# Performance work log

Measured on AMD Instinct MI355X. Metric: run time of the kernel, lower is better.

The kernel has to match this reference:

```python
import jax, jax.numpy as jnp
import numpy as np

N = 8192   # nodes
F = 16     # node features (col 0 = signal, last 3 = xyz)
H = 64     # hidden
G = 256    # number of graphs (segments)
EPS = 1e-3 # keras LayerNormalization default epsilon


def setup_inputs() -> dict:
    key = jax.random.key(0)
    ks = jax.random.split(key, 10)
    s = 0.05
    X = jax.random.normal(ks[0], (N, F), jnp.float32)
    # dense pre-normalized adjacency (spektral GCNConv expects normalized A)
    A = jax.random.uniform(ks[1], (N, N), jnp.float32) * (1.0 / N)
    I = jnp.sort(jax.random.randint(ks[2], (N,), 0, G)).astype(jnp.int32)
    W0 = jax.random.normal(ks[3], (F, H), jnp.float32) * s
    b0 = jnp.zeros((H,), jnp.float32)
    g0 = jnp.ones((H,), jnp.float32)
    be0 = jnp.zeros((H,), jnp.float32)
    W1 = jax.random.normal(ks[4], (H, H), jnp.float32) * s
    b1 = jnp.zeros((H,), jnp.float32)
    g1 = jnp.ones((H,), jnp.float32)
    be1 = jnp.zeros((H,), jnp.float32)
    Wf = jax.random.normal(ks[5], (H, H), jnp.float32) * s
    bf = jnp.zeros((H,), jnp.float32)
    Wa = jax.random.normal(ks[6], (H, H), jnp.float32) * s
    ba = jnp.zeros((H,), jnp.float32)
    Wout = jax.random.normal(ks[7], (H + 3, 3), jnp.float32) * s
    bout = jnp.zeros((3,), jnp.float32)
    return dict(X=X, A=A, I=I, W0=W0, b0=b0, g0=g0, be0=be0,
                W1=W1, b1=b1, g1=g1, be1=be1,
                Wf=Wf, bf=bf, Wa=Wa, ba=ba, Wout=Wout, bout=bout)


def _layer_norm(x, gamma, beta):
    m = jnp.mean(x, axis=-1, keepdims=True)
    v = jnp.mean(jnp.square(x - m), axis=-1, keepdims=True)
    return (x - m) * jax.lax.rsqrt(v + EPS) * gamma + beta


def reference(X, A, I, W0, b0, g0, be0, W1, b1, g1, be1, Wf, bf, Wa, ba, Wout, bout):
    I = I.astype(jnp.int32)
    # GCN layer 0: relu(A @ X @ W0 + b0) -> LayerNorm
    h0 = _layer_norm(jax.nn.relu(A @ (X @ W0) + b0), g0, be0)
    # GCN layer 1 + LayerNorm + residual (i > 0)
    h = _layer_norm(jax.nn.relu(A @ (h0 @ W1) + b1), g1, be1) + h0
    # GlobalAttentionPool: Dense features * sigmoid-gated attention, segment-summed per graph
    feat = h @ Wf + bf                       # [N, H]
    attn = jax.nn.sigmoid(h @ Wa + ba)       # [N, H]
    g = jax.ops.segment_sum(feat * attn, I, num_segments=G)  # [G, H]
    # Signal-weighted barycentre via segment-softmax over log1p(relu(signal))
    z = jnp.log1p(jax.nn.relu(X[:, 0]))                       # [N]
    zmax = jax.ops.segment_max(z, I, num_segments=G)          # [G]
    zexp = jnp.exp(z - zmax[I])                               # [N]
    zsum = jax.ops.segment_sum(zexp, I, num_segments=G)       # [G]
    w = zexp / zsum[I]                                        # [N]
    bary = jax.ops.segment_sum(w[:, None] * X[:, -3:], I, num_segments=G)  # [G, 3]
    return jnp.concatenate([g, bary], axis=-1) @ Wout + bout  # [G, 3]
```

## Files before the change

kernel.cpp:

```cpp
#include <hip/hip_runtime.h>
#include <hip/hip_bf16.h>
#include <math.h>

#define NN 8192
#define FF 16
#define HH 64
#define GG 256
#define LN_EPS 1e-3f
#define KSPLIT 16
#define KC (NN / KSPLIT)

typedef __bf16 bf16x8 __attribute__((ext_vector_type(8)));
typedef float  floatx4 __attribute__((ext_vector_type(4)));

__global__ __launch_bounds__(256)
void k1_xw0(const float* __restrict__ X,
            const float* __restrict__ W0,
            const int* __restrict__ I,
            __hip_bfloat16* __restrict__ Zt0,
            float* __restrict__ zarr,
            unsigned int* __restrict__ zmax_bits) {
    __shared__ float Xs[64][17];
    __shared__ float W0s[16][64];
    const int t  = threadIdx.x;
    const int i0 = blockIdx.x * 64;
    {
        const int r = t >> 2, c = (t & 3) * 4;
        const float4 v = *reinterpret_cast<const float4*>(&X[(size_t)(i0 + r) * FF + c]);
        Xs[r][c + 0] = v.x; Xs[r][c + 1] = v.y; Xs[r][c + 2] = v.z; Xs[r][c + 3] = v.w;
        const float4 w = *reinterpret_cast<const float4*>(&W0[t * 4]);
        const int wr = t >> 4, wc = (t & 15) * 4;
        W0s[wr][wc + 0] = w.x; W0s[wr][wc + 1] = w.y; W0s[wr][wc + 2] = w.z; W0s[wr][wc + 3] = w.w;
    }
    __syncthreads();
    const int i  = t & 63;
    const int n0 = (t >> 6) * 16;
    float s[16];
#pragma unroll
    for (int j = 0; j < 16; ++j) s[j] = 0.f;
#pragma unroll
    for (int m = 0; m < FF; ++m) {
        const float hv = Xs[i][m];
        const float4* wrow = reinterpret_cast<const float4*>(&W0s[m][n0]);
        const float4 w0 = wrow[0], w1 = wrow[1], w2 = wrow[2], w3 = wrow[3];
        s[0]  += hv * w0.x; s[1]  += hv * w0.y; s[2]  += hv * w0.z; s[3]  += hv * w0.w;
        s[4]  += hv * w1.x; s[5]  += hv * w1.y; s[6]  += hv * w1.z; s[7]  += hv * w1.w;
        s[8]  += hv * w2.x; s[9]  += hv * w2.y; s[10] += hv * w2.z; s[11] += hv * w2.w;
        s[12] += hv * w3.x; s[13] += hv * w3.y; s[14] += hv * w3.z; s[15] += hv * w3.w;
    }
#pragma unroll
    for (int j = 0; j < 16; ++j)
        Zt0[(size_t)(n0 + j) * NN + i0 + i] = __float2bfloat16(s[j]);

    if (t < 64) {
        const float z = log1pf(fmaxf(Xs[t][0], 0.f));
        zarr[i0 + t] = z;
        atomicMax(&zmax_bits[I[i0 + t]], __float_as_uint(z));
    }
}

__global__ __launch_bounds__(256)
void k_gemm_split(const float* __restrict__ A,
                  const __hip_bfloat16* __restrict__ Zt,
                  float* __restrict__ Cp) {
    const int tid  = threadIdx.x;
    const int wave = tid >> 6;
    const int lane = tid & 63;
    const int l16  = lane & 15;
    const int quad = lane >> 4;
    const int rb   = blockIdx.x & 127;
    const int kb   = blockIdx.x >> 7;
    const int row0 = rb * 64;
    const int k0   = kb * KC;

    const float* aptr = A + (size_t)(row0 + wave * 16 + l16) * NN + k0 + quad * 8;
    const __hip_bfloat16* bp0 = Zt + (size_t)(0 * 16 + l16) * NN + k0 + quad * 8;
    const __hip_bfloat16* bp1 = Zt + (size_t)(1 * 16 + l16) * NN + k0 + quad * 8;
    const __hip_bfloat16* bp2 = Zt + (size_t)(2 * 16 + l16) * NN + k0 + quad * 8;
    const __hip_bfloat16* bp3 = Zt + (size_t)(3 * 16 + l16) * NN + k0 + quad * 8;

    floatx4 acc0 = {0.f,0.f,0.f,0.f}, acc1 = {0.f,0.f,0.f,0.f};
    floatx4 acc2 = {0.f,0.f,0.f,0.f}, acc3 = {0.f,0.f,0.f,0.f};

#pragma unroll 4
    for (int k = 0; k < KC; k += 32) {
        const float4 a0 = *reinterpret_cast<const float4*>(aptr + k);
        const float4 a1 = *reinterpret_cast<const float4*>(aptr + k + 4);
        bf16x8 af;
        af[0] = (__bf16)a0.x; af[1] = (__bf16)a0.y;
        af[2] = (__bf16)a0.z; af[3] = (__bf16)a0.w;
        af[4] = (__bf16)a1.x; af[5] = (__bf16)a1.y;
        af[6] = (__bf16)a1.z; af[7] = (__bf16)a1.w;
        const bf16x8 b0 = *reinterpret_cast<const bf16x8*>(bp0 + k);
        const bf16x8 b1 = *reinterpret_cast<const bf16x8*>(bp1 + k);
        const bf16x8 b2 = *reinterpret_cast<const bf16x8*>(bp2 + k);
        const bf16x8 b3 = *reinterpret_cast<const bf16x8*>(bp3 + k);
        acc0 = __builtin_amdgcn_mfma_f32_16x16x32_bf16(af, b0, acc0, 0, 0, 0);
        acc1 = __builtin_amdgcn_mfma_f32_16x16x32_bf16(af, b1, acc1, 0, 0, 0);
        acc2 = __builtin_amdgcn_mfma_f32_16x16x32_bf16(af, b2, acc2, 0, 0, 0);
        acc3 = __builtin_amdgcn_mfma_f32_16x16x32_bf16(af, b3, acc3, 0, 0, 0);
    }

    float* cp = Cp + ((size_t)kb * NN + row0 + wave * 16 + quad * 4) * HH + l16;
#pragma unroll
    for (int r = 0; r < 4; ++r) {
        cp[(size_t)r * HH +  0] = acc0[r];
        cp[(size_t)r * HH + 16] = acc1[r];
        cp[(size_t)r * HH + 32] = acc2[r];
        cp[(size_t)r * HH + 48] = acc3[r];
    }
}

__global__ __launch_bounds__(256)
void k_red_ln(const float* __restrict__ Cp,
              const float* __restrict__ bias,
              const float* __restrict__ gamma,
              const float* __restrict__ beta,
              const float* __restrict__ resid,
              float* __restrict__ out) {
    const int tid = threadIdx.x;
    const int row = tid >> 4;
    const int c0  = (tid & 15) * 4;
    const size_t grow = (size_t)(blockIdx.x * 16 + row);

    float4 a = {0.f, 0.f, 0.f, 0.f};
#pragma unroll
    for (int kb = 0; kb < KSPLIT; ++kb) {
        const float4 v = *reinterpret_cast<const float4*>(&Cp[((size_t)kb * NN + grow) * HH + c0]);
        a.x += v.x; a.y += v.y; a.z += v.z; a.w += v.w;
    }
    const float4 b4 = *reinterpret_cast<const float4*>(&bias[c0]);
    float v[4] = { fmaxf(a.x + b4.x, 0.f), fmaxf(a.y + b4.y, 0.f),
                   fmaxf(a.z + b4.z, 0.f), fmaxf(a.w + b4.w, 0.f) };
    float s = 0.f, ss = 0.f;
#pragma unroll
    for (int j = 0; j < 4; ++j) { s += v[j]; ss += v[j] * v[j]; }
#pragma unroll
    for (int m = 1; m < 16; m <<= 1) {
        s  += __shfl_xor(s,  m, 64);
        ss += __shfl_xor(ss, m, 64);
    }
    const float mean = s * (1.f / 64.f);
    const float var  = fmaxf(ss * (1.f / 64.f) - mean * mean, 0.f);
    const float inv  = rsqrtf(var + LN_EPS);
    const float4 g4  = *reinterpret_cast<const float4*>(&gamma[c0]);
    const float4 be4 = *reinterpret_cast<const float4*>(&beta[c0]);
    float4 o;
    o.x = (v[0] - mean) * inv * g4.x + be4.x;
    o.y = (v[1] - mean) * inv * g4.y + be4.y;
    o.z = (v[2] - mean) * inv * g4.z + be4.z;
    o.w = (v[3] - mean) * inv * g4.w + be4.w;
    if (resid) {
        const float4 r4 = *reinterpret_cast<const float4*>(&resid[grow * HH + c0]);
        o.x += r4.x; o.y += r4.y; o.z += r4.z; o.w += r4.w;
    }
    *reinterpret_cast<float4*>(&out[grow * HH + c0]) = o;
}

__global__ __launch_bounds__(256)
void k3_hw1(const float* __restrict__ h0,
            const float* __restrict__ W1,
            __hip_bfloat16* __restrict__ Zt1) {
    __shared__ float Hs[64][65];
    __shared__ float Ws[64][64];
    const int t  = threadIdx.x;
    const int i0 = blockIdx.x * 64;
#pragma unroll
    for (int p = 0; p < 4; ++p) {
        const int idx = p * 256 + t;
        const int r = idx >> 4, c = (idx & 15) * 4;
        const float4 v = *reinterpret_cast<const float4*>(&h0[(size_t)(i0 + r) * HH + c]);
        Hs[r][c + 0] = v.x; Hs[r][c + 1] = v.y; Hs[r][c + 2] = v.z; Hs[r][c + 3] = v.w;
        const float4 w = *reinterpret_cast<const float4*>(&W1[(size_t)r * HH + c]);
        Ws[r][c + 0] = w.x; Ws[r][c + 1] = w.y; Ws[r][c + 2] = w.z; Ws[r][c + 3] = w.w;
    }
    __syncthreads();
    const int i  = t & 63;
    const int n0 = (t >> 6) * 16;
    float s[16];
#pragma unroll
    for (int j = 0; j < 16; ++j) s[j] = 0.f;
#pragma unroll
    for (int m = 0; m < HH; ++m) {
        const float hv = Hs[i][m];
        const float4* wrow = reinterpret_cast<const float4*>(&Ws[m][n0]);
        const float4 w0 = wrow[0], w1 = wrow[1], w2 = wrow[2], w3 = wrow[3];
        s[0]  += hv * w0.x; s[1]  += hv * w0.y; s[2]  += hv * w0.z; s[3]  += hv * w0.w;
        s[4]  += hv * w1.x; s[5]  += hv * w1.y; s[6]  += hv * w1.z; s[7]  += hv * w1.w;
        s[8]  += hv * w2.x; s[9]  += hv * w2.y; s[10] += hv * w2.z; s[11] += hv * w2.w;
        s[12] += hv * w3.x; s[13] += hv * w3.y; s[14] += hv * w3.z; s[15] += hv * w3.w;
    }
#pragma unroll
    for (int j = 0; j < 16; ++j)
        Zt1[(size_t)(n0 + j) * NN + i0 + i] = __float2bfloat16(s[j]);
}

__global__ __launch_bounds__(256)
void k5_pool(const float* __restrict__ h,
             const float* __restrict__ Wf, const float* __restrict__ bfv,
             const float* __restrict__ Wa, const float* __restrict__ bav,
             const int* __restrict__ I,
             const float* __restrict__ X,
             const float* __restrict__ zarr,
             const float* __restrict__ zmax,
             float* __restrict__ g,
             float* __restrict__ zsum,
             float* __restrict__ baryn) {
    __shared__ float hrow[4][64];
    const int w = threadIdx.x >> 6, l = threadIdx.x & 63;
    const int node = blockIdx.x * 4 + w;
    hrow[w][l] = h[(size_t)node * HH + l];
    __syncthreads();
    float sf = bfv[l], sa = bav[l];
#pragma unroll 8
    for (int m = 0; m < HH; ++m) {
        const float hv = hrow[w][m];
        sf += hv * Wf[m * HH + l];
        sa += hv * Wa[m * HH + l];
    }
    const float attn = 1.f / (1.f + expf(-sa));
    const int seg = I[node];
    atomicAdd(&g[(size_t)seg * HH + l], sf * attn);

    if (l < 4) {
        const float ze = expf(zarr[node] - zmax[seg]);
        if (l == 0) atomicAdd(&zsum[seg], ze);
        else        atomicAdd(&baryn[seg * 3 + (l - 1)], ze * X[(size_t)node * FF + 12 + l]);
    }
}

__global__ __launch_bounds__(256)
void k7_out(const float* __restrict__ g,
            const float* __restrict__ zsum,
            const float* __restrict__ baryn,
            const float* __restrict__ Wout,
            const float* __restrict__ bout,
            float* __restrict__ out) {
    const int w = threadIdx.x >> 6, lane = threadIdx.x & 63;
    const int gi = blockIdx.x * 4 + w;
    const float vg = g[(size_t)gi * HH + lane];
    const float zs = zsum[gi];
    const float invz = (zs > 0.f) ? (1.f / zs) : 0.f;
    const float extra = (lane < 3) ? baryn[gi * 3 + lane] * invz : 0.f;
#pragma unroll
    for (int d = 0; d < 3; ++d) {
        float p = vg * Wout[lane * 3 + d];
        if (lane < 3) p += extra * Wout[(64 + lane) * 3 + d];
#pragma unroll
        for (int m = 1; m < 64; m <<= 1) p += __shfl_xor(p, m, 64);
        if (lane == 0) out[gi * 3 + d] = p + bout[d];
    }
}

extern "C" void kernel_launch(void* const* d_in, const int* in_sizes, int n_in,
                              void* d_out, int out_size, void* d_ws, size_t ws_size,
                              hipStream_t stream) {
    const float* X   = (const float*)d_in[0];
    const float* A   = (const float*)d_in[1];
    const int*   I   = (const int*)d_in[2];
    const float* W0  = (const float*)d_in[3];
    const float* b0  = (const float*)d_in[4];
    const float* g0  = (const float*)d_in[5];
    const float* be0 = (const float*)d_in[6];
    const float* W1  = (const float*)d_in[7];
    const float* b1  = (const float*)d_in[8];
    const float* g1  = (const float*)d_in[9];
    const float* be1 = (const float*)d_in[10];
    const float* Wf  = (const float*)d_in[11];
    const float* bfv = (const float*)d_in[12];
    const float* Wa  = (const float*)d_in[13];
    const float* bav = (const float*)d_in[14];
    const float* Wo  = (const float*)d_in[15];
    const float* bo  = (const float*)d_in[16];

    char* ws = (char*)d_ws;
    float* Cp = (float*)ws;
    __hip_bfloat16* Zt0 = (__hip_bfloat16*)(ws + (32u << 20));
    __hip_bfloat16* Zt1 = (__hip_bfloat16*)(ws + (33u << 20));
    float* h0   = (float*)(ws + (34u << 20));
    float* h    = (float*)(ws + (36u << 20));
    float* zarr = (float*)(ws + (38u << 20));
    float* acc  = (float*)(ws + (38u << 20) + (64u << 10));
    float* g     = acc;
    float* zmax  = acc + GG * HH;
    float* zsum  = zmax + GG;
    float* baryn = zsum + GG;
    const size_t memset_bytes = (size_t)(GG * HH + GG + GG + GG * 3) * sizeof(float);

    hipMemsetAsync(acc, 0, memset_bytes, stream);

    k1_xw0<<<128, 256, 0, stream>>>(X, W0, I, Zt0, zarr, (unsigned int*)zmax);
    k_gemm_split<<<2048, 256, 0, stream>>>(A, Zt0, Cp);
    k_red_ln<<<512, 256, 0, stream>>>(Cp, b0, g0, be0, nullptr, h0);
    k3_hw1<<<128, 256, 0, stream>>>(h0, W1, Zt1);
    k_gemm_split<<<2048, 256, 0, stream>>>(A, Zt1, Cp);
    k_red_ln<<<512, 256, 0, stream>>>(Cp, b1, g1, be1, h0, h);
    k5_pool<<<2048, 256, 0, stream>>>(h, Wf, bfv, Wa, bav, I, X, zarr, zmax, g, zsum, baryn);
    k7_out<<<64, 256, 0, stream>>>(g, zsum, baryn, Wo, bo, (float*)d_out);
}
```

Baseline: 582.6 us.

## Replace split-K GEMM with LDS double-buffered full-K GEMM per row block

The A@Z GEMM drops split-K with partial-sum buffers and instead has each block own 16 rows over the full K range. The block stages A tiles through XOR-swizzled, double-buffered LDS so the four waves (one per 16 output columns) share each A load rather than each loading A separately. This removes the partial-sum write/read traffic and lets the LayerNorm kernel read a single C. The trade-offs are fewer blocks (512), a long serial K loop per block with a barrier at every stage, and only one MFMA accumulator chain per wave, which may limit latency hiding on the memory-bound 256MB A read.

```diff
diff --git a/kernel.cpp b/kernel.cpp
--- a/kernel.cpp
+++ b/kernel.cpp
@@ -7,8 +7,8 @@
 #define HH 64
 #define GG 256
 #define LN_EPS 1e-3f
-#define KSPLIT 16
-#define KC (NN / KSPLIT)
+#define BK 256
+#define KSTAGES (NN / BK)
 
 typedef __bf16 bf16x8 __attribute__((ext_vector_type(8)));
 typedef float  floatx4 __attribute__((ext_vector_type(4)));
@@ -60,75 +60,87 @@
 }
 
 __global__ __launch_bounds__(256)
-void k_gemm_split(const float* __restrict__ A,
-                  const __hip_bfloat16* __restrict__ Zt,
-                  float* __restrict__ Cp) {
-    const int tid  = threadIdx.x;
-    const int wave = tid >> 6;
-    const int lane = tid & 63;
+void k_gemm_lds(const float* __restrict__ A,
+                const __hip_bfloat16* __restrict__ Zt,
+                float* __restrict__ C) {
+    __shared__ float Ab[2][16][256];
+    const int t    = threadIdx.x;
+    const int w    = t >> 6;
+    const int lane = t & 63;
     const int l16  = lane & 15;
     const int quad = lane >> 4;
-    const int rb   = blockIdx.x & 127;
-    const int kb   = blockIdx.x >> 7;
-    const int row0 = rb * 64;
-    const int k0   = kb * KC;
-
-    const float* aptr = A + (size_t)(row0 + wave * 16 + l16) * NN + k0 + quad * 8;
-    const __hip_bfloat16* bp0 = Zt + (size_t)(0 * 16 + l16) * NN + k0 + quad * 8;
-    const __hip_bfloat16* bp1 = Zt + (size_t)(1 * 16 + l16) * NN + k0 + quad * 8;
-    const __hip_bfloat16* bp2 = Zt + (size_t)(2 * 16 + l16) * NN + k0 + quad * 8;
-    const __hip_bfloat16* bp3 = Zt + (size_t)(3 * 16 + l16) * NN + k0 + quad * 8;
-
-    floatx4 acc0 = {0.f,0.f,0.f,0.f}, acc1 = {0.f,0.f,0.f,0.f};
-    floatx4 acc2 = {0.f,0.f,0.f,0.f}, acc3 = {0.f,0.f,0.f,0.f};
-
-#pragma unroll 4
-    for (int k = 0; k < KC; k += 32) {
-        const float4 a0 = *reinterpret_cast<const float4*>(aptr + k);
-        const float4 a1 = *reinterpret_cast<const float4*>(aptr + k + 4);
-        bf16x8 af;
-        af[0] = (__bf16)a0.x; af[1] = (__bf16)a0.y;
-        af[2] = (__bf16)a0.z; af[3] = (__bf16)a0.w;
-        af[4] = (__bf16)a1.x; af[5] = (__bf16)a1.y;
-        af[6] = (__bf16)a1.z; af[7] = (__bf16)a1.w;
-        const bf16x8 b0 = *reinterpret_cast<const bf16x8*>(bp0 + k);
-        const bf16x8 b1 = *reinterpret_cast<const bf16x8*>(bp1 + k);
-        const bf16x8 b2 = *reinterpret_cast<const bf16x8*>(bp2 + k);
-        const bf16x8 b3 = *reinterpret_cast<const bf16x8*>(bp3 + k);
-        acc0 = __builtin_amdgcn_mfma_f32_16x16x32_bf16(af, b0, acc0, 0, 0, 0);
-        acc1 = __builtin_amdgcn_mfma_f32_16x16x32_bf16(af, b1, acc1, 0, 0, 0);
-        acc2 = __builtin_amdgcn_mfma_f32_16x16x32_bf16(af, b2, acc2, 0, 0, 0);
-        acc3 = __builtin_amdgcn_mfma_f32_16x16x32_bf16(af, b3, acc3, 0, 0, 0);
-    }
-
-    float* cp = Cp + ((size_t)kb * NN + row0 + wave * 16 + quad * 4) * HH + l16;
-#pragma unroll
-    for (int r = 0; r < 4; ++r) {
-        cp[(size_t)r * HH +  0] = acc0[r];
-        cp[(size_t)r * HH + 16] = acc1[r];
-        cp[(size_t)r * HH + 32] = acc2[r];
-        cp[(size_t)r * HH + 48] = acc3[r];
-    }
-}
-
-__global__ __launch_bounds__(256)
-void k_red_ln(const float* __restrict__ Cp,
-              const float* __restrict__ bias,
-              const float* __restrict__ gamma,
-              const float* __restrict__ beta,
-              const float* __restrict__ resid,
-              float* __restrict__ out) {
+    const int row0 = blockIdx.x * 16;
+    const int sc   = lane * 4;
+    const int swz  = (l16 & 7) << 2;
+
+    const __hip_bfloat16* bp = Zt + (size_t)(w * 16 + l16) * NN + quad * 8;
+    const float* arow = A + (size_t)row0 * NN;
+
+    floatx4 acc = {0.f, 0.f, 0.f, 0.f};
+
+    {
+        float4 st[4];
+#pragma unroll
+        for (int j = 0; j < 4; ++j)
+            st[j] = *reinterpret_cast<const float4*>(arow + (size_t)(j * 4 + w) * NN + sc);
+#pragma unroll
+        for (int j = 0; j < 4; ++j) {
+            const int r = j * 4 + w;
+            *reinterpret_cast<float4*>(&Ab[0][r][sc ^ ((r & 7) << 2)]) = st[j];
+        }
+    }
+    __syncthreads();
+
+    int cur = 0;
+    for (int s = 0; s < KSTAGES; ++s) {
+        float4 nx[4];
+        const bool pf = (s + 1 < KSTAGES);
+        if (pf) {
+#pragma unroll
+            for (int j = 0; j < 4; ++j)
+                nx[j] = *reinterpret_cast<const float4*>(
+                    arow + (size_t)(j * 4 + w) * NN + (size_t)(s + 1) * BK + sc);
+        }
+#pragma unroll
+        for (int kk = 0; kk < 8; ++kk) {
+            const int c = kk * 32 + quad * 8;
+            const float4 alo = *reinterpret_cast<const float4*>(&Ab[cur][l16][(c    ) ^ swz]);
+            const float4 ahi = *reinterpret_cast<const float4*>(&Ab[cur][l16][(c + 4) ^ swz]);
+            bf16x8 af;
+            af[0]=(__bf16)alo.x; af[1]=(__bf16)alo.y; af[2]=(__bf16)alo.z; af[3]=(__bf16)alo.w;
+            af[4]=(__bf16)ahi.x; af[5]=(__bf16)ahi.y; af[6]=(__bf16)ahi.z; af[7]=(__bf16)ahi.w;
+            const bf16x8 b = *reinterpret_cast<const bf16x8*>(bp + (size_t)s * BK + kk * 32);
+            acc = __builtin_amdgcn_mfma_f32_16x16x32_bf16(af, b, acc, 0, 0, 0);
+        }
+        if (pf) {
+#pragma unroll
+            for (int j = 0; j < 4; ++j) {
+                const int r = j * 4 + w;
+                *reinterpret_cast<float4*>(&Ab[cur ^ 1][r][sc ^ ((r & 7) << 2)]) = nx[j];
+            }
+        }
+        __syncthreads();
+        cur ^= 1;
+    }
+
+#pragma unroll
+    for (int r = 0; r < 4; ++r)
+        C[(size_t)(row0 + quad * 4 + r) * HH + w * 16 + l16] = acc[r];
+}
+
+__global__ __launch_bounds__(256)
+void k_ln(const float* __restrict__ C,
+          const float* __restrict__ bias,
+          const float* __restrict__ gamma,
+          const float* __restrict__ beta,
+          const float* __restrict__ resid,
+          float* __restrict__ out) {
     const int tid = threadIdx.x;
     const int row = tid >> 4;
     const int c0  = (tid & 15) * 4;
     const size_t grow = (size_t)(blockIdx.x * 16 + row);
 
-    float4 a = {0.f, 0.f, 0.f, 0.f};
-#pragma unroll
-    for (int kb = 0; kb < KSPLIT; ++kb) {
-        const float4 v = *reinterpret_cast<const float4*>(&Cp[((size_t)kb * NN + grow) * HH + c0]);
-        a.x += v.x; a.y += v.y; a.z += v.z; a.w += v.w;
-    }
+    const float4 a = *reinterpret_cast<const float4*>(&C[grow * HH + c0]);
     const float4 b4 = *reinterpret_cast<const float4*>(&bias[c0]);
     float v[4] = { fmaxf(a.x + b4.x, 0.f), fmaxf(a.y + b4.y, 0.f),
                    fmaxf(a.z + b4.z, 0.f), fmaxf(a.w + b4.w, 0.f) };
@@ -274,13 +286,13 @@
     const float* bo  = (const float*)d_in[16];
 
     char* ws = (char*)d_ws;
-    float* Cp = (float*)ws;
-    __hip_bfloat16* Zt0 = (__hip_bfloat16*)(ws + (32u << 20));
-    __hip_bfloat16* Zt1 = (__hip_bfloat16*)(ws + (33u << 20));
-    float* h0   = (float*)(ws + (34u << 20));
-    float* h    = (float*)(ws + (36u << 20));
-    float* zarr = (float*)(ws + (38u << 20));
-    float* acc  = (float*)(ws + (38u << 20) + (64u << 10));
+    float* C    = (float*)ws;
+    __hip_bfloat16* Zt0 = (__hip_bfloat16*)(ws + (2u << 20));
+    __hip_bfloat16* Zt1 = (__hip_bfloat16*)(ws + (3u << 20));
+    float* h0   = (float*)(ws + (4u << 20));
+    float* h    = (float*)(ws + (6u << 20));
+    float* zarr = (float*)(ws + (8u << 20));
+    float* acc  = (float*)(ws + (8u << 20) + (64u << 10));
     float* g     = acc;
     float* zmax  = acc + GG * HH;
     float* zsum  = zmax + GG;
@@ -290,11 +302,11 @@
     hipMemsetAsync(acc, 0, memset_bytes, stream);
 
     k1_xw0<<<128, 256, 0, stream>>>(X, W0, I, Zt0, zarr, (unsigned int*)zmax);
-    k_gemm_split<<<2048, 256, 0, stream>>>(A, Zt0, Cp);
-    k_red_ln<<<512, 256, 0, stream>>>(Cp, b0, g0, be0, nullptr, h0);
+    k_gemm_lds<<<512, 256, 0, stream>>>(A, Zt0, C);
+    k_ln<<<512, 256, 0, stream>>>(C, b0, g0, be0, nullptr, h0);
     k3_hw1<<<128, 256, 0, stream>>>(h0, W1, Zt1);
-    k_gemm_split<<<2048, 256, 0, stream>>>(A, Zt1, Cp);
-    k_red_ln<<<512, 256, 0, stream>>>(Cp, b1, g1, be1, h0, h);
+    k_gemm_lds<<<512, 256, 0, stream>>>(A, Zt1, C);
+    k_ln<<<512, 256, 0, stream>>>(C, b1, g1, be1, h0, h);
     k5_pool<<<2048, 256, 0, stream>>>(h, Wf, bfv, Wa, bav, I, X, zarr, zmax, g, zsum, baryn);
     k7_out<<<64, 256, 0, stream>>>(g, zsum, baryn, Wo, bo, (float*)d_out);
 }
```

After: 684.0 us. 1.17x slower.
